# Kernel optimization log

Measured on AMD Instinct MI355X. Metric: run time of the kernel, lower is better.

The kernel has to match this reference:

```python
import jax, jax.numpy as jnp
import numpy as np

N, IN_DIM, HID, OUT_DIM = 200000, 64, 128, 64
E = 3200000


def setup_inputs() -> dict:
    key = jax.random.key(0)
    ks = jax.random.split(key, 24)
    s_in = 1.0 / np.sqrt(IN_DIM)
    s_h = 1.0 / np.sqrt(HID)
    inp = {
        "x": jax.random.normal(ks[0], (N, IN_DIM), jnp.float32),
        "edge_index": jax.random.randint(ks[1], (2, E), 0, N, jnp.int64),
        "batch": jnp.zeros((N,), jnp.int64),
        # input projections W_{i,f,c,o}: [IN_DIM, HID]
        "W_i": jax.random.normal(ks[2], (IN_DIM, HID), jnp.float32) * s_in,
        "W_f": jax.random.normal(ks[3], (IN_DIM, HID), jnp.float32) * s_in,
        "W_c": jax.random.normal(ks[4], (IN_DIM, HID), jnp.float32) * s_in,
        "W_o": jax.random.normal(ks[5], (IN_DIM, HID), jnp.float32) * s_in,
        # ChebConv(K=1) weights on H: Theta0 [HID, HID] + conv bias [HID]
        "Wg_i": jax.random.normal(ks[6], (HID, HID), jnp.float32) * s_h,
        "Wg_f": jax.random.normal(ks[7], (HID, HID), jnp.float32) * s_h,
        "Wg_c": jax.random.normal(ks[8], (HID, HID), jnp.float32) * s_h,
        "Wg_o": jax.random.normal(ks[9], (HID, HID), jnp.float32) * s_h,
        "bg_i": jax.random.normal(ks[10], (HID,), jnp.float32) * 0.02,
        "bg_f": jax.random.normal(ks[11], (HID,), jnp.float32) * 0.02,
        "bg_c": jax.random.normal(ks[12], (HID,), jnp.float32) * 0.02,
        "bg_o": jax.random.normal(ks[13], (HID,), jnp.float32) * 0.02,
        # peephole weights w_c_* [1, HID] and gate biases b_* [1, HID]
        "wc_i": jax.random.normal(ks[14], (1, HID), jnp.float32) * 0.02,
        "wc_f": jax.random.normal(ks[15], (1, HID), jnp.float32) * 0.02,
        "wc_o": jax.random.normal(ks[16], (1, HID), jnp.float32) * 0.02,
        "b_i": jax.random.normal(ks[17], (1, HID), jnp.float32) * 0.02,
        "b_f": jax.random.normal(ks[18], (1, HID), jnp.float32) * 0.02,
        "b_c": jax.random.normal(ks[19], (1, HID), jnp.float32) * 0.02,
        "b_o": jax.random.normal(ks[20], (1, HID), jnp.float32) * 0.02,
        # final fc: [HID, OUT_DIM]
        "fc_W": jax.random.normal(ks[21], (HID, OUT_DIM), jnp.float32) * s_h,
        "fc_b": jax.random.normal(ks[22], (OUT_DIM,), jnp.float32) * 0.02,
    }
    return inp


def _gclstm_step(x, H, C, W_i, W_f, W_c, W_o, Wg_i, Wg_f, Wg_c, Wg_o,
                 bg_i, bg_f, bg_c, bg_o, wc_i, wc_f, wc_o, b_i, b_f, b_c, b_o):
    # ChebConv with K=1: T_0(L) = I, so conv(H) = H @ Theta0 + bias (edge_index is a no-op)
    conv = lambda Wg, bg: H @ Wg + bg
    i = jax.nn.sigmoid(x @ W_i + conv(Wg_i, bg_i) + wc_i * C + b_i)
    f = jax.nn.sigmoid(x @ W_f + conv(Wg_f, bg_f) + wc_f * C + b_f)
    t = jnp.tanh(x @ W_c + conv(Wg_c, bg_c) + b_c)
    C_new = f * C + i * t
    o = jax.nn.sigmoid(x @ W_o + conv(Wg_o, bg_o) + wc_o * C_new + b_o)
    H_new = o * jnp.tanh(C_new)
    return H_new, C_new


def reference(x, edge_index, batch, W_i, W_f, W_c, W_o, Wg_i, Wg_f, Wg_c, Wg_o,
              bg_i, bg_f, bg_c, bg_o, wc_i, wc_f, wc_o, b_i, b_f, b_c, b_o,
              fc_W, fc_b):
    # H=None, C=None in the original call -> zeros init, single LSTM step
    H0 = jnp.zeros((x.shape[0], W_i.shape[1]), x.dtype)
    C0 = jnp.zeros_like(H0)
    H, C = _gclstm_step(x, H0, C0, W_i, W_f, W_c, W_o, Wg_i, Wg_f, Wg_c, Wg_o,
                        bg_i, bg_f, bg_c, bg_o, wc_i, wc_f, wc_o,
                        b_i, b_f, b_c, b_o)
    return H @ fc_W + fc_b  # [N, OUT_DIM]
```

## Files before the change

kernel.cpp:

```cpp
#include <hip/hip_runtime.h>


typedef __attribute__((ext_vector_type(8))) short short8;
typedef __attribute__((ext_vector_type(4))) short short4_t;
typedef __attribute__((ext_vector_type(4))) float f32x4;

#define N_ROWS 200000
#define IN_DIM 64
#define HID 128
#define OUT_DIM 64

#define WFRAG_ELEMS (24 * 2 * 64 * 8)
#define FCFRAG_OFF  49152
#define FCFRAG_ELEMS (4 * 4 * 64 * 8)
#define BIAS_OFF    65536

__device__ __forceinline__ short f2bf(float f) {
  unsigned u = __float_as_uint(f);
  u += 0x7FFFu + ((u >> 16) & 1u);
  return (short)(u >> 16);
}
__device__ __forceinline__ float fexp2(float z) { return __builtin_amdgcn_exp2f(z); }
__device__ __forceinline__ float frcp(float z)  { return __builtin_amdgcn_rcpf(z); }
__device__ __forceinline__ float fsigmoid(float z) {
  return frcp(1.0f + fexp2(-1.44269504f * z));
}
__device__ __forceinline__ float ftanh(float z) {
  return 1.0f - 2.0f * frcp(1.0f + fexp2(2.88539008f * z));
}

__global__ void repack_kernel(const float* __restrict__ W_i, const float* __restrict__ W_c,
                              const float* __restrict__ W_o, const float* __restrict__ fc_W,
                              const float* __restrict__ bg_i, const float* __restrict__ bg_c,
                              const float* __restrict__ bg_o,
                              const float* __restrict__ b_i, const float* __restrict__ b_c,
                              const float* __restrict__ b_o, const float* __restrict__ wc_o,
                              const float* __restrict__ fc_b,
                              short* __restrict__ wfrag, short* __restrict__ fcfrag,
                              float* __restrict__ bias) {
  int tid = blockIdx.x * blockDim.x + threadIdx.x;
  const int total1 = WFRAG_ELEMS;
  const int total2 = FCFRAG_ELEMS;
  for (int e = tid; e < total1 + total2 + HID + OUT_DIM; e += gridDim.x * blockDim.x) {
    if (e < total1) {
      int j = e & 7, lane = (e >> 3) & 63, s = (e >> 9) & 1, t = e >> 10;
      int q = lane >> 4, cidx = lane & 15;
      int gate = t >> 3;
      int h = (t & 7) * 16 + cidx;
      int feat = 32 * s + 8 * q + j;
      const float* W = (gate == 0) ? W_i : ((gate == 1) ? W_c : W_o);
      wfrag[e] = f2bf(W[feat * HID + h]);
    } else if (e < total1 + total2) {
      int e2 = e - total1;
      int j = e2 & 7, lane = (e2 >> 3) & 63, s = (e2 >> 9) & 3, t = e2 >> 11;
      int q = lane >> 4, cidx = lane & 15;
      int od = 16 * t + cidx;
      int hid = 32 * s + 8 * q + j;
      fcfrag[e2] = f2bf(fc_W[hid * OUT_DIM + od]);
    } else if (e < total1 + total2 + HID) {
      int h = e - total1 - total2;
      bias[h]           = bg_i[h] + b_i[h];
      bias[HID + h]     = bg_c[h] + b_c[h];
      bias[2 * HID + h] = bg_o[h] + b_o[h];
      bias[3 * HID + h] = wc_o[h];
    } else {
      int h2 = e - total1 - total2 - HID;
      bias[4 * HID + h2] = fc_b[h2];
    }
  }
}

__global__ __launch_bounds__(256) void gclstm_fused(
    const float* __restrict__ x, const short* __restrict__ wfrag,
    const short* __restrict__ fcfrag, const float* __restrict__ bias,
    float* __restrict__ out) {
  __shared__ short Hlds[4 * 32 * 128];
  const int lane = threadIdx.x & 63;
  const int wslot = threadIdx.x >> 6;
  const int wid = blockIdx.x * 4 + wslot;
  const int row0 = wid * 32;
  if (row0 >= N_ROWS) return;
  const int q = lane >> 4, cidx = lane & 15;
  short* hbase = Hlds + wslot * (32 * 128);
  const int swz = (cidx & 7) << 3;

  short8 bx[2][2];
#pragma unroll
  for (int m = 0; m < 2; ++m) {
    const float* xr = x + (size_t)(row0 + 16 * m + cidx) * IN_DIM + 8 * q;
#pragma unroll
    for (int s = 0; s < 2; ++s) {
      f32x4 f0 = *(const f32x4*)(xr + 32 * s);
      f32x4 f1 = *(const f32x4*)(xr + 32 * s + 4);
      short8 v;
      v[0] = f2bf(f0[0]); v[1] = f2bf(f0[1]); v[2] = f2bf(f0[2]); v[3] = f2bf(f0[3]);
      v[4] = f2bf(f1[0]); v[5] = f2bf(f1[1]); v[6] = f2bf(f1[2]); v[7] = f2bf(f1[3]);
      bx[m][s] = v;
    }
  }

  const float* Bi  = bias;
  const float* Bc  = bias + HID;
  const float* Bo  = bias + 2 * HID;
  const float* Wco = bias + 3 * HID;
  const float* Fcb = bias + 4 * HID;
  const f32x4 zero4 = {0.f, 0.f, 0.f, 0.f};

#pragma unroll
  for (int g = 0; g < 8; ++g) {
    f32x4 acc[3][2];
#pragma unroll
    for (int a = 0; a < 3; ++a) { acc[a][0] = zero4; acc[a][1] = zero4; }
#pragma unroll
    for (int s = 0; s < 2; ++s) {
      short8 ai = *(const short8*)(wfrag + (((g     ) * 2 + s) * 64 + lane) * 8);
      short8 ac = *(const short8*)(wfrag + (((g +  8) * 2 + s) * 64 + lane) * 8);
      short8 ao = *(const short8*)(wfrag + (((g + 16) * 2 + s) * 64 + lane) * 8);
#pragma unroll
      for (int m = 0; m < 2; ++m) {
        acc[0][m] = __builtin_amdgcn_mfma_f32_16x16x32_bf16(ai, bx[m][s], acc[0][m], 0, 0, 0);
        acc[1][m] = __builtin_amdgcn_mfma_f32_16x16x32_bf16(ac, bx[m][s], acc[1][m], 0, 0, 0);
        acc[2][m] = __builtin_amdgcn_mfma_f32_16x16x32_bf16(ao, bx[m][s], acc[2][m], 0, 0, 0);
      }
    }
    const int h0 = g * 16 + 4 * q;
    f32x4 vbi = *(const f32x4*)(Bi + h0);
    f32x4 vbc = *(const f32x4*)(Bc + h0);
    f32x4 vbo = *(const f32x4*)(Bo + h0);
    f32x4 vwc = *(const f32x4*)(Wco + h0);
#pragma unroll
    for (int m = 0; m < 2; ++m) {
      short4_t hw;
#pragma unroll
      for (int r = 0; r < 4; ++r) {
        float gi = fsigmoid(acc[0][m][r] + vbi[r]);
        float gt = ftanh(acc[1][m][r] + vbc[r]);
        float C  = gi * gt;
        float go = fsigmoid(acc[2][m][r] + vbo[r] + vwc[r] * C);
        hw[r] = f2bf(go * ftanh(C));
      }
      const int xrow = 16 * m + cidx;
      *(short4_t*)(hbase + (((xrow * 128 + h0) ^ swz))) = hw;
    }
  }

  f32x4 oacc[4][2];
#pragma unroll
  for (int t = 0; t < 4; ++t) { oacc[t][0] = zero4; oacc[t][1] = zero4; }
#pragma unroll
  for (int s = 0; s < 4; ++s) {
    short8 bh[2];
#pragma unroll
    for (int m = 0; m < 2; ++m) {
      const int xrow = 16 * m + cidx;
      bh[m] = *(const short8*)(hbase + (((xrow * 128 + 32 * s + 8 * q) ^ swz)));
    }
#pragma unroll
    for (int t = 0; t < 4; ++t) {
      short8 af = *(const short8*)(fcfrag + ((t * 4 + s) * 64 + lane) * 8);
#pragma unroll
      for (int m = 0; m < 2; ++m)
        oacc[t][m] = __builtin_amdgcn_mfma_f32_16x16x32_bf16(af, bh[m], oacc[t][m], 0, 0, 0);
    }
  }

#pragma unroll
  for (int t = 0; t < 4; ++t) {
    const int od0 = 16 * t + 4 * q;
    f32x4 fb = *(const f32x4*)(Fcb + od0);
#pragma unroll
    for (int m = 0; m < 2; ++m) {
      f32x4 v = oacc[t][m] + fb;
      *(f32x4*)(out + (size_t)(row0 + 16 * m + cidx) * OUT_DIM + od0) = v;
    }
  }
}

extern "C" void kernel_launch(void* const* d_in, const int* in_sizes, int n_in,
                              void* d_out, int out_size, void* d_ws, size_t ws_size,
                              hipStream_t stream) {
  (void)in_sizes; (void)n_in; (void)out_size; (void)ws_size;
  const float* x    = (const float*)d_in[0];
  const float* W_i  = (const float*)d_in[3];
  const float* W_c  = (const float*)d_in[5];
  const float* W_o  = (const float*)d_in[6];
  const float* bg_i = (const float*)d_in[11];
  const float* bg_c = (const float*)d_in[13];
  const float* bg_o = (const float*)d_in[14];
  const float* wc_o = (const float*)d_in[17];
  const float* b_i  = (const float*)d_in[18];
  const float* b_c  = (const float*)d_in[20];
  const float* b_o  = (const float*)d_in[21];
  const float* fc_W = (const float*)d_in[22];
  const float* fc_b = (const float*)d_in[23];

  short* wfrag  = (short*)d_ws;
  short* fcfrag = (short*)((char*)d_ws + FCFRAG_OFF);
  float* bias   = (float*)((char*)d_ws + BIAS_OFF);

  repack_kernel<<<dim3(64), dim3(256), 0, stream>>>(
      W_i, W_c, W_o, fc_W, bg_i, bg_c, bg_o, b_i, b_c, b_o, wc_o, fc_b,
      wfrag, fcfrag, bias);

  const int nchunks = (N_ROWS + 31) / 32;
  const int nwg = (nchunks + 3) / 4;
  gclstm_fused<<<dim3(nwg), dim3(256), 0, stream>>>(
      x, wfrag, fcfrag, bias, (float*)d_out);
}
```

Baseline: 55.78 us.

## Widen per-wave tile to 64 rows and interleave FC GEMM with gate computation

Each wave now processes 64 rows instead of 32, so every weight fragment load feeds four MFMAs per gate instead of two. The final FC MMA is interleaved per 32-wide hidden slice into the gate loop, using a small double-buffered LDS tile in place of a full 32x128 H buffer. Biases are folded into the accumulator initialisation. Blocks shrink to 128 threads with launch bounds (128,2), and register pressure rises from the larger accumulator arrays (oacc 4x4, acc 3x4), which may lower occupancy.

```diff
diff --git a/kernel.cpp b/kernel.cpp
--- a/kernel.cpp
+++ b/kernel.cpp
@@ -70,32 +70,31 @@
   }
 }
 
-__global__ __launch_bounds__(256) void gclstm_fused(
+__global__ __launch_bounds__(128, 2) void gclstm_fused(
     const float* __restrict__ x, const short* __restrict__ wfrag,
     const short* __restrict__ fcfrag, const float* __restrict__ bias,
     float* __restrict__ out) {
-  __shared__ short Hlds[4 * 32 * 128];
+  __shared__ short Hlds[2 * 2 * 64 * 32];
   const int lane = threadIdx.x & 63;
   const int wslot = threadIdx.x >> 6;
-  const int wid = blockIdx.x * 4 + wslot;
-  const int row0 = wid * 32;
+  const int wid = blockIdx.x * 2 + wslot;
+  const int row0 = wid * 64;
   if (row0 >= N_ROWS) return;
   const int q = lane >> 4, cidx = lane & 15;
-  short* hbase = Hlds + wslot * (32 * 128);
-  const int swz = (cidx & 7) << 3;
-
-  short8 bx[2][2];
-#pragma unroll
-  for (int m = 0; m < 2; ++m) {
+  short* hb0 = Hlds + wslot * (2 * 64 * 32);
+
+  short8 bx[4][2];
+#pragma unroll
+  for (int m = 0; m < 4; ++m) {
     const float* xr = x + (size_t)(row0 + 16 * m + cidx) * IN_DIM + 8 * q;
 #pragma unroll
-    for (int s = 0; s < 2; ++s) {
-      f32x4 f0 = *(const f32x4*)(xr + 32 * s);
-      f32x4 f1 = *(const f32x4*)(xr + 32 * s + 4);
+    for (int sk = 0; sk < 2; ++sk) {
+      f32x4 f0 = *(const f32x4*)(xr + 32 * sk);
+      f32x4 f1 = *(const f32x4*)(xr + 32 * sk + 4);
       short8 v;
       v[0] = f2bf(f0[0]); v[1] = f2bf(f0[1]); v[2] = f2bf(f0[2]); v[3] = f2bf(f0[3]);
       v[4] = f2bf(f1[0]); v[5] = f2bf(f1[1]); v[6] = f2bf(f1[2]); v[7] = f2bf(f1[3]);
-      bx[m][s] = v;
+      bx[m][sk] = v;
     }
   }
 
@@ -104,62 +103,69 @@
   const float* Bo  = bias + 2 * HID;
   const float* Wco = bias + 3 * HID;
   const float* Fcb = bias + 4 * HID;
-  const f32x4 zero4 = {0.f, 0.f, 0.f, 0.f};
-
-#pragma unroll
-  for (int g = 0; g < 8; ++g) {
-    f32x4 acc[3][2];
-#pragma unroll
-    for (int a = 0; a < 3; ++a) { acc[a][0] = zero4; acc[a][1] = zero4; }
-#pragma unroll
-    for (int s = 0; s < 2; ++s) {
-      short8 ai = *(const short8*)(wfrag + (((g     ) * 2 + s) * 64 + lane) * 8);
-      short8 ac = *(const short8*)(wfrag + (((g +  8) * 2 + s) * 64 + lane) * 8);
-      short8 ao = *(const short8*)(wfrag + (((g + 16) * 2 + s) * 64 + lane) * 8);
-#pragma unroll
-      for (int m = 0; m < 2; ++m) {
-        acc[0][m] = __builtin_amdgcn_mfma_f32_16x16x32_bf16(ai, bx[m][s], acc[0][m], 0, 0, 0);
-        acc[1][m] = __builtin_amdgcn_mfma_f32_16x16x32_bf16(ac, bx[m][s], acc[1][m], 0, 0, 0);
-        acc[2][m] = __builtin_amdgcn_mfma_f32_16x16x32_bf16(ao, bx[m][s], acc[2][m], 0, 0, 0);
+
+  f32x4 oacc[4][4];
+#pragma unroll
+  for (int t = 0; t < 4; ++t) {
+    f32x4 fb = *(const f32x4*)(Fcb + 16 * t + 4 * q);
+#pragma unroll
+    for (int m = 0; m < 4; ++m) oacc[t][m] = fb;
+  }
+
+#pragma unroll
+  for (int s = 0; s < 4; ++s) {
+    short* hb = hb0 + (s & 1) * (64 * 32);
+#pragma unroll
+    for (int gg = 0; gg < 2; ++gg) {
+      const int g = 2 * s + gg;
+      const int h0 = g * 16 + 4 * q;
+      f32x4 vbi = *(const f32x4*)(Bi + h0);
+      f32x4 vbc = *(const f32x4*)(Bc + h0);
+      f32x4 vbo = *(const f32x4*)(Bo + h0);
+      f32x4 vwc = *(const f32x4*)(Wco + h0);
+      f32x4 acc[3][4];
+#pragma unroll
+      for (int m = 0; m < 4; ++m) { acc[0][m] = vbi; acc[1][m] = vbc; acc[2][m] = vbo; }
+#pragma unroll
+      for (int sk = 0; sk < 2; ++sk) {
+        short8 ai = *(const short8*)(wfrag + (((g     ) * 2 + sk) * 64 + lane) * 8);
+        short8 ac = *(const short8*)(wfrag + (((g +  8) * 2 + sk) * 64 + lane) * 8);
+        short8 ao = *(const short8*)(wfrag + (((g + 16) * 2 + sk) * 64 + lane) * 8);
+#pragma unroll
+        for (int m = 0; m < 4; ++m) {
+          acc[0][m] = __builtin_amdgcn_mfma_f32_16x16x32_bf16(ai, bx[m][sk], acc[0][m], 0, 0, 0);
+          acc[1][m] = __builtin_amdgcn_mfma_f32_16x16x32_bf16(ac, bx[m][sk], acc[1][m], 0, 0, 0);
+          acc[2][m] = __builtin_amdgcn_mfma_f32_16x16x32_bf16(ao, bx[m][sk], acc[2][m], 0, 0, 0);
+        }
       }
-    }
-    const int h0 = g * 16 + 4 * q;
-    f32x4 vbi = *(const f32x4*)(Bi + h0);
-    f32x4 vbc = *(const f32x4*)(Bc + h0);
-    f32x4 vbo = *(const f32x4*)(Bo + h0);
-    f32x4 vwc = *(const f32x4*)(Wco + h0);
-#pragma unroll
-    for (int m = 0; m < 2; ++m) {
-      short4_t hw;
-#pragma unroll
-      for (int r = 0; r < 4; ++r) {
-        float gi = fsigmoid(acc[0][m][r] + vbi[r]);
-        float gt = ftanh(acc[1][m][r] + vbc[r]);
-        float C  = gi * gt;
-        float go = fsigmoid(acc[2][m][r] + vbo[r] + vwc[r] * C);
-        hw[r] = f2bf(go * ftanh(C));
+#pragma unroll
+      for (int m = 0; m < 4; ++m) {
+        short4_t hw;
+#pragma unroll
+        for (int r = 0; r < 4; ++r) {
+          float gi = fsigmoid(acc[0][m][r]);
+          float gt = ftanh(acc[1][m][r]);
+          float C  = gi * gt;
+          float go = fsigmoid(acc[2][m][r] + vwc[r] * C);
+          hw[r] = f2bf(go * ftanh(C));
+        }
+        const int xrow = 16 * m + cidx;
+        const int l0 = (16 * gg + 4 * q) ^ ((xrow & 3) << 3);
+        *(short4_t*)(hb + xrow * 32 + l0) = hw;
       }
+    }
+    short8 bh[4];
+#pragma unroll
+    for (int m = 0; m < 4; ++m) {
       const int xrow = 16 * m + cidx;
-      *(short4_t*)(hbase + (((xrow * 128 + h0) ^ swz))) = hw;
-    }
-  }
-
-  f32x4 oacc[4][2];
-#pragma unroll
-  for (int t = 0; t < 4; ++t) { oacc[t][0] = zero4; oacc[t][1] = zero4; }
-#pragma unroll
-  for (int s = 0; s < 4; ++s) {
-    short8 bh[2];
-#pragma unroll
-    for (int m = 0; m < 2; ++m) {
-      const int xrow = 16 * m + cidx;
-      bh[m] = *(const short8*)(hbase + (((xrow * 128 + 32 * s + 8 * q) ^ swz)));
+      const int l0 = (8 * q) ^ ((xrow & 3) << 3);
+      bh[m] = *(const short8*)(hb + xrow * 32 + l0);
     }
 #pragma unroll
     for (int t = 0; t < 4; ++t) {
       short8 af = *(const short8*)(fcfrag + ((t * 4 + s) * 64 + lane) * 8);
 #pragma unroll
-      for (int m = 0; m < 2; ++m)
+      for (int m = 0; m < 4; ++m)
         oacc[t][m] = __builtin_amdgcn_mfma_f32_16x16x32_bf16(af, bh[m], oacc[t][m], 0, 0, 0);
     }
   }
@@ -167,11 +173,9 @@
 #pragma unroll
   for (int t = 0; t < 4; ++t) {
     const int od0 = 16 * t + 4 * q;
-    f32x4 fb = *(const f32x4*)(Fcb + od0);
-#pragma unroll
-    for (int m = 0; m < 2; ++m) {
-      f32x4 v = oacc[t][m] + fb;
-      *(f32x4*)(out + (size_t)(row0 + 16 * m + cidx) * OUT_DIM + od0) = v;
+#pragma unroll
+    for (int m = 0; m < 4; ++m) {
+      *(f32x4*)(out + (size_t)(row0 + 16 * m + cidx) * OUT_DIM + od0) = oacc[t][m];
     }
   }
 }
@@ -202,8 +206,8 @@
       W_i, W_c, W_o, fc_W, bg_i, bg_c, bg_o, b_i, b_c, b_o, wc_o, fc_b,
       wfrag, fcfrag, bias);
 
-  const int nchunks = (N_ROWS + 31) / 32;
-  const int nwg = (nchunks + 3) / 4;
-  gclstm_fused<<<dim3(nwg), dim3(256), 0, stream>>>(
+  const int nwaves = N_ROWS / 64;
+  const int nwg = (nwaves + 1) / 2;
+  gclstm_fused<<<dim3(nwg), dim3(128), 0, stream>>>(
       x, wfrag, fcfrag, bias, (float*)d_out);
 }
```

Result: slower. 62.42 us (+11.9%).
